# Kernel optimization log

Measured on AMD Instinct MI355X. Metric: run time of the kernel, lower is better.

Reference implementation:

```python
import jax, jax.numpy as jnp
import numpy as np

N_HEAD = 16

def setup_inputs() -> dict:
    key = jax.random.key(0)
    k1, k2, k3 = jax.random.split(key, 3)
    B, T, C = 2, 2048, 2048
    x = jax.random.normal(k1, (B, T, C), dtype=jnp.float32)
    # torch Linear weights are [out, in]; init with small scale for stability
    w_attn = jax.random.normal(k2, (3 * C, C), dtype=jnp.float32) * 0.02
    b_attn = jnp.zeros((3 * C,), dtype=jnp.float32)
    w_proj = jax.random.normal(k3, (C, C), dtype=jnp.float32) * 0.02
    b_proj = jnp.zeros((C,), dtype=jnp.float32)
    return {"x": x, "w_attn": w_attn, "b_attn": b_attn, "w_proj": w_proj, "b_proj": b_proj}

def reference(x, w_attn, b_attn, w_proj, b_proj):
    B, T, C = x.shape
    nh = N_HEAD
    hs = C // nh
    # fused QKV projection (torch Linear: x @ W^T + b)
    qkv = x @ w_attn.T + b_attn                      # [B, T, 3C]
    q, k, v = jnp.split(qkv, 3, axis=2)
    # [B, nh, T, hs]
    q = q.reshape(B, T, nh, hs).transpose(0, 2, 1, 3)
    k = k.reshape(B, T, nh, hs).transpose(0, 2, 1, 3)
    v = v.reshape(B, T, nh, hs).transpose(0, 2, 1, 3)
    # causal scaled dot-product attention
    scale = 1.0 / jnp.sqrt(jnp.asarray(hs, dtype=x.dtype))
    logits = jnp.einsum("bhqd,bhkd->bhqk", q, k) * scale  # [B, nh, T, T]
    causal = jnp.tril(jnp.ones((T, T), dtype=bool))
    logits = jnp.where(causal, logits, jnp.finfo(logits.dtype).min)
    attn = jax.nn.softmax(logits, axis=-1)
    y = jnp.einsum("bhqk,bhkd->bhqd", attn, v)       # [B, nh, T, hs]
    y = y.transpose(0, 2, 1, 3).reshape(B, T, C)
    # output projection (resid_dropout is identity in eval / p=0)
    y = y @ w_proj.T + b_proj
    return y
```

## Files before the change

### kernel.cpp

```cpp
#include <hip/hip_runtime.h>
#include <stdint.h>

typedef __bf16 bf16_t;
typedef __bf16 bf16x8 __attribute__((ext_vector_type(8)));
typedef float f32x4 __attribute__((ext_vector_type(4)));
typedef unsigned short us16x8 __attribute__((ext_vector_type(8)));

#define MFMA16(a, b, c) __builtin_amdgcn_mfma_f32_16x16x32_bf16(a, b, c, 0, 0, 0)
#define BAR() __builtin_amdgcn_s_barrier()
#define PRIO1() __builtin_amdgcn_s_setprio(1)
#define PRIO0() __builtin_amdgcn_s_setprio(0)
#define LGKM0()                                        \
  do {                                                 \
    asm volatile("s_waitcnt lgkmcnt(0)" ::: "memory"); \
    __builtin_amdgcn_sched_barrier(0);                 \
  } while (0)
#define VMCNT(n)                                          \
  do {                                                    \
    asm volatile("s_waitcnt vmcnt(" #n ")" ::: "memory"); \
    __builtin_amdgcn_sched_barrier(0);                    \
  } while (0)

__device__ __forceinline__ void stage16(const bf16_t* g, bf16_t* l) {
  __builtin_amdgcn_global_load_lds((__attribute__((address_space(1))) void*)g,
                                   (__attribute__((address_space(3))) void*)l, 16, 0, 0);
}

__global__ __launch_bounds__(256) void cvt_f32_to_bf16(const float* __restrict__ in,
                                                       bf16_t* __restrict__ out, int n8) {
  int i = blockIdx.x * 256 + threadIdx.x;
  if (i >= n8) return;
  const f32x4* p = (const f32x4*)(in + (size_t)i * 8);
  f32x4 a = p[0], b = p[1];
  bf16x8 o;
  o[0] = (bf16_t)a[0]; o[1] = (bf16_t)a[1]; o[2] = (bf16_t)a[2]; o[3] = (bf16_t)a[3];
  o[4] = (bf16_t)b[0]; o[5] = (bf16_t)b[1]; o[6] = (bf16_t)b[2]; o[7] = (bf16_t)b[3];
  *(bf16x8*)(out + (size_t)i * 8) = o;
}

template <int OUT_BF16>
__global__ __launch_bounds__(512, 2) void gemm_nt_p2(const bf16_t* __restrict__ A,
                                                     const bf16_t* __restrict__ B,
                                                     const float* __restrict__ bias,
                                                     void* __restrict__ Cout,
                                                     int M, int N, int K) {
  __shared__ bf16_t SA[2 * 2 * 256 * 32];
  __shared__ bf16_t SB[2 * 2 * 128 * 32];
  const int tid = threadIdx.x;
  const int l = tid & 63, w = tid >> 6;
  const int l15 = l & 15, l4 = l >> 4;
  const int wm = w >> 1, wn = w & 1;
  const int nbm = M >> 8;
  const int nwg = gridDim.x;
  const int bid = blockIdx.x;
  const int wg = (bid & 7) * (nwg >> 3) + (bid >> 3);
  const int bn = wg / nbm, bm = wg % nbm;

  const int sA0 = tid, sA1 = 512 + tid;
  const int rA0 = sA0 >> 2, rA1 = sA1 >> 2, rB = tid >> 2;
  const int cA0 = ((sA0 & 3) ^ ((rA0 >> 1) & 3)) << 3;
  const int cA1 = ((sA1 & 3) ^ ((rA1 >> 1) & 3)) << 3;
  const int cB = ((tid & 3) ^ ((rB >> 1) & 3)) << 3;
  const bf16_t* gA0 = A + (size_t)(bm * 256 + rA0) * K + cA0;
  const bf16_t* gA1 = A + (size_t)(bm * 256 + rA1) * K + cA1;
  const bf16_t* gB = B + (size_t)(bn * 128 + rB) * K + cB;

  int aoff[4], boff[4];
#pragma unroll
  for (int mi = 0; mi < 4; ++mi) {
    int r = wm * 64 + mi * 16 + l15;
    aoff[mi] = r * 32 + ((l4 ^ ((r >> 1) & 3)) << 3);
  }
#pragma unroll
  for (int ni = 0; ni < 4; ++ni) {
    int r = wn * 64 + ni * 16 + l15;
    boff[ni] = r * 32 + ((l4 ^ ((r >> 1) & 3)) << 3);
  }

  f32x4 acc[4][4] = {};

  auto STAGE = [&](int tau, int h, int buf) {
    const int koff = tau * 64 + h * 32;
    stage16(gA0 + koff, SA + buf * 16384 + h * 8192 + sA0 * 8);
    stage16(gA1 + koff, SA + buf * 16384 + h * 8192 + sA1 * 8);
    stage16(gB + koff, SB + buf * 8192 + h * 4096 + tid * 8);
  };

  auto PHASE = [&](int buf, int h, int tauS, int hS, int bufS) {
    bf16x8 aR[4], bR[4];
#pragma unroll
    for (int mi = 0; mi < 4; ++mi)
      aR[mi] = *(const bf16x8*)(SA + buf * 16384 + h * 8192 + aoff[mi]);
#pragma unroll
    for (int ni = 0; ni < 4; ++ni)
      bR[ni] = *(const bf16x8*)(SB + buf * 8192 + h * 4096 + boff[ni]);
    STAGE(tauS, hS, bufS);
    VMCNT(6);
    BAR();
    LGKM0();
    PRIO1();
#pragma unroll
    for (int mi = 0; mi < 4; ++mi)
#pragma unroll
      for (int ni = 0; ni < 4; ++ni) acc[mi][ni] = MFMA16(aR[mi], bR[ni], acc[mi][ni]);
    PRIO0();
    BAR();
  };

  const int nk = K >> 6;
  STAGE(0, 0, 0);
  STAGE(0, 1, 0);
  STAGE(1, 0, 1);
  VMCNT(6);
  BAR();

  for (int t = 0; t < nk; t += 2) {
    const int t1a = (t + 1 < nk) ? t + 1 : nk - 1;
    const int t2a = (t + 2 < nk) ? t + 2 : nk - 1;
    const int t3a = (t + 3 < nk) ? t + 3 : nk - 1;
    PHASE(0, 0, t1a, 1, 1);
    PHASE(0, 1, t2a, 0, 0);
    PHASE(1, 0, t2a, 1, 0);
    PHASE(1, 1, t3a, 0, 1);
  }
  VMCNT(0);

  const int rbase = bm * 256 + wm * 64 + (l4 << 2);
  const int cbase = bn * 128 + wn * 64 + l15;
#pragma unroll
  for (int ni = 0; ni < 4; ++ni) {
    float bv = bias[cbase + ni * 16];
#pragma unroll
    for (int mi = 0; mi < 4; ++mi)
#pragma unroll
      for (int r = 0; r < 4; ++r) {
        float v = acc[mi][ni][r] + bv;
        size_t off = (size_t)(rbase + mi * 16 + r) * N + (cbase + ni * 16);
        if (OUT_BF16) ((bf16_t*)Cout)[off] = (bf16_t)v;
        else ((float*)Cout)[off] = v;
      }
  }
}

__global__ __launch_bounds__(256, 2) void attn_fwd(const bf16_t* __restrict__ qkv,
                                                   bf16_t* __restrict__ att) {
  __shared__ bf16_t Kt[64 * 128];
  __shared__ bf16_t Vt[128 * 64];
  __shared__ bf16_t Pw[4][16 * 64];

  int bid = blockIdx.x;
  int pair = bid >> 5, bh = bid & 31;
  int h = bh & 15, b = bh >> 4;
  int tid = threadIdx.x;
  int l = tid & 63, w = tid >> 6;
  int l15 = l & 15, l4 = l >> 4, l7 = l & 7;
  const size_t LD = 6144;
  const bf16_t* base = qkv + (size_t)b * 2048 * LD;

#pragma unroll 1
  for (int phase = 0; phase < 2; ++phase) {
    int qt = phase ? 31 - pair : pair;
    int q0 = qt << 6;
    int wq0 = q0 + w * 16;

    bf16x8 qf[4];
#pragma unroll
    for (int kk = 0; kk < 4; ++kk)
      qf[kk] = *(const bf16x8*)(base + (size_t)(wq0 + l15) * LD + h * 128 + kk * 32 + l4 * 8);

    f32x4 acc[8] = {};
    float mrow[4], lrow[4];
#pragma unroll
    for (int r = 0; r < 4; ++r) { mrow[r] = -1e30f; lrow[r] = 0.f; }

    int nkt = qt + 1;
    for (int kt = 0; kt < nkt; ++kt) {
      int kb = kt << 6;
      const bf16_t* vg = base + (size_t)kb * LD + 4096 + h * 128;
      us16x8 va[2], vb[2];
#pragma unroll
      for (int p = 0; p < 2; ++p) {
        int g = p * 256 + tid;
        int kv = (g >> 4) << 1;
        int d0 = (g & 15) << 3;
        va[p] = *(const us16x8*)(vg + (size_t)kv * LD + d0);
        vb[p] = *(const us16x8*)(vg + (size_t)(kv + 1) * LD + d0);
      }
      const bf16_t* kg = base + (size_t)kb * LD + 2048 + h * 128;
#pragma unroll
      for (int i = 0; i < 4; ++i) {
        int e = i * 256 + tid;
        int row = e >> 4, blk = e & 15;
        int src = (blk ^ (row & 7)) << 3;
        stage16(kg + (size_t)row * LD + src, Kt + e * 8);
      }
#pragma unroll
      for (int p = 0; p < 2; ++p) {
        int g = p * 256 + tid;
        int kv = (g >> 4) << 1;
        int d0 = (g & 15) << 3;
        int k8 = kv >> 3, kr = kv & 7;
#pragma unroll
        for (int j = 0; j < 8; ++j) {
          int d = d0 + j;
          int swz = k8 ^ ((d ^ (d >> 3)) & 7);
          unsigned pack = (unsigned)va[p][j] | ((unsigned)vb[p][j] << 16);
          *(unsigned*)(&Vt[d * 64 + swz * 8 + kr]) = pack;
        }
      }
      __syncthreads();

      {
        f32x4 s[4] = {};
        __builtin_amdgcn_s_setprio(1);
#pragma unroll
        for (int kk = 0; kk < 4; ++kk) {
          int blk = (kk * 4 + l4) ^ l7;
#pragma unroll
          for (int n = 0; n < 4; ++n) {
            bf16x8 kf = *(const bf16x8*)(Kt + (n * 16 + l15) * 128 + blk * 8);
            s[n] = MFMA16(qf[kk], kf, s[n]);
          }
        }
        __builtin_amdgcn_s_setprio(0);

        const float sc = 0.08838834764831845f;
        bool needMask = (kb + 63) > wq0;
        float scf[4];
#pragma unroll
        for (int r = 0; r < 4; ++r) {
          int q = wq0 + (l4 << 2) + r;
#pragma unroll
          for (int n = 0; n < 4; ++n) {
            float v = s[n][r] * sc;
            if (needMask && (kb + n * 16 + l15) > q) v = -1e30f;
            s[n][r] = v;
          }
          float mx = fmaxf(fmaxf(s[0][r], s[1][r]), fmaxf(s[2][r], s[3][r]));
          mx = fmaxf(mx, __shfl_xor(mx, 1));
          mx = fmaxf(mx, __shfl_xor(mx, 2));
          mx = fmaxf(mx, __shfl_xor(mx, 4));
          mx = fmaxf(mx, __shfl_xor(mx, 8));
          float mn = fmaxf(mrow[r], mx);
          float sf = __expf(mrow[r] - mn);
          mrow[r] = mn;
          scf[r] = sf;
          float rs = 0.f;
#pragma unroll
          for (int n = 0; n < 4; ++n) {
            float pv = __expf(s[n][r] - mn);
            s[n][r] = pv;
            rs += pv;
          }
          rs += __shfl_xor(rs, 1);
          rs += __shfl_xor(rs, 2);
          rs += __shfl_xor(rs, 4);
          rs += __shfl_xor(rs, 8);
          lrow[r] = lrow[r] * sf + rs;
        }
#pragma unroll
        for (int nd = 0; nd < 8; ++nd)
#pragma unroll
          for (int r = 0; r < 4; ++r)
            acc[nd][r] *= scf[r];
#pragma unroll
        for (int n = 0; n < 4; ++n) {
          int cb8 = n * 2 + (l15 >> 3);
#pragma unroll
          for (int r = 0; r < 4; ++r) {
            int row = (l4 << 2) + r;
            Pw[w][row * 64 + ((cb8 ^ (row & 7)) << 3) + l7] = (bf16_t)s[n][r];
          }
        }
        __builtin_amdgcn_s_setprio(1);
#pragma unroll
        for (int kk2 = 0; kk2 < 2; ++kk2) {
          bf16x8 pa = *(const bf16x8*)(&Pw[w][l15 * 64 + (((kk2 * 4 + l4) ^ l7) << 3)]);
#pragma unroll
          for (int nd = 0; nd < 8; ++nd) {
            int d = nd * 16 + l15;
            int swz = (kk2 * 4 + l4) ^ ((d ^ (d >> 3)) & 7);
            bf16x8 bv = *(const bf16x8*)(&Vt[d * 64 + swz * 8]);
            acc[nd] = MFMA16(pa, bv, acc[nd]);
          }
        }
        __builtin_amdgcn_s_setprio(0);
      }
      __syncthreads();
    }

#pragma unroll
    for (int r = 0; r < 4; ++r) {
      float inv = 1.0f / lrow[r];
      size_t ro = (size_t)(b * 2048 + wq0 + (l4 << 2) + r) * 2048 + h * 128;
#pragma unroll
      for (int nd = 0; nd < 8; ++nd)
        att[ro + nd * 16 + l15] = (bf16_t)(acc[nd][r] * inv);
    }
  }
}

extern "C" void kernel_launch(void* const* d_in, const int* in_sizes, int n_in,
                              void* d_out, int out_size, void* d_ws, size_t ws_size,
                              hipStream_t stream) {
  (void)in_sizes; (void)n_in; (void)out_size; (void)ws_size;
  const float* x = (const float*)d_in[0];
  const float* w_attn = (const float*)d_in[1];
  const float* b_attn = (const float*)d_in[2];
  const float* w_proj = (const float*)d_in[3];
  const float* b_proj = (const float*)d_in[4];
  float* out = (float*)d_out;

  char* ws = (char*)d_ws;
  bf16_t* xb  = (bf16_t*)(ws);
  bf16_t* wab = (bf16_t*)(ws + 16777216);
  bf16_t* wpb = (bf16_t*)(ws + 41943040);
  bf16_t* qkv = (bf16_t*)(ws + 50331648);
  bf16_t* att = xb;

  cvt_f32_to_bf16<<<4096, 256, 0, stream>>>(x, xb, 1048576);
  cvt_f32_to_bf16<<<6144, 256, 0, stream>>>(w_attn, wab, 1572864);
  cvt_f32_to_bf16<<<2048, 256, 0, stream>>>(w_proj, wpb, 524288);

  gemm_nt_p2<1><<<768, 512, 0, stream>>>(xb, wab, b_attn, qkv, 4096, 6144, 2048);

  attn_fwd<<<512, 256, 0, stream>>>(qkv, att);

  gemm_nt_p2<0><<<256, 512, 0, stream>>>(att, wpb, b_proj, out, 4096, 2048, 2048);
}
```

Baseline: 310.0 us.

## Replace GEMM with 128x128-tile, 256-thread kernel using quadrant-phased MFMA schedule

Swaps the 256x128-tile, 512-thread GEMM for a 128x128-tile, 256-thread kernel with BK=32 double buffering. Each K-tile is split into four MFMA quadrant phases, with LDS reads and global-to-LDS staging interleaved between them. The smaller tiles double the workgroup count and cut LDS use, so three blocks can share a CU and occupancy and load balance should improve. In exchange there is less data reuse per tile and more barriers per K step. The LDS swizzle is also dropped, which may add bank conflicts.

```diff
diff --git a/kernel.cpp b/kernel.cpp
--- a/kernel.cpp
+++ b/kernel.cpp
@@ -39,93 +39,111 @@
 }
 
 template <int OUT_BF16>
-__global__ __launch_bounds__(512, 2) void gemm_nt_p2(const bf16_t* __restrict__ A,
+__global__ __launch_bounds__(256, 3) void gemm_nt_c4(const bf16_t* __restrict__ A,
                                                      const bf16_t* __restrict__ B,
                                                      const float* __restrict__ bias,
                                                      void* __restrict__ Cout,
                                                      int M, int N, int K) {
-  __shared__ bf16_t SA[2 * 2 * 256 * 32];
-  __shared__ bf16_t SB[2 * 2 * 128 * 32];
+  __shared__ bf16_t SA[2 * 2 * 64 * 32];
+  __shared__ bf16_t SB[2 * 2 * 64 * 32];
   const int tid = threadIdx.x;
   const int l = tid & 63, w = tid >> 6;
   const int l15 = l & 15, l4 = l >> 4;
   const int wm = w >> 1, wn = w & 1;
-  const int nbm = M >> 8;
+  const int nbm = M >> 7;
   const int nwg = gridDim.x;
   const int bid = blockIdx.x;
   const int wg = (bid & 7) * (nwg >> 3) + (bid >> 3);
   const int bn = wg / nbm, bm = wg % nbm;
 
-  const int sA0 = tid, sA1 = 512 + tid;
-  const int rA0 = sA0 >> 2, rA1 = sA1 >> 2, rB = tid >> 2;
-  const int cA0 = ((sA0 & 3) ^ ((rA0 >> 1) & 3)) << 3;
-  const int cA1 = ((sA1 & 3) ^ ((rA1 >> 1) & 3)) << 3;
-  const int cB = ((tid & 3) ^ ((rB >> 1) & 3)) << 3;
-  const bf16_t* gA0 = A + (size_t)(bm * 256 + rA0) * K + cA0;
-  const bf16_t* gA1 = A + (size_t)(bm * 256 + rA1) * K + cA1;
-  const bf16_t* gB = B + (size_t)(bn * 128 + rB) * K + cB;
-
-  int aoff[4], boff[4];
-#pragma unroll
-  for (int mi = 0; mi < 4; ++mi) {
-    int r = wm * 64 + mi * 16 + l15;
-    aoff[mi] = r * 32 + ((l4 ^ ((r >> 1) & 3)) << 3);
-  }
-#pragma unroll
-  for (int ni = 0; ni < 4; ++ni) {
-    int r = wn * 64 + ni * 16 + l15;
-    boff[ni] = r * 32 + ((l4 ^ ((r >> 1) & 3)) << 3);
-  }
+  const int srow = tid >> 2, scol = (tid & 3) << 3;
+  const bf16_t* gA0 = A + (size_t)(bm * 128 + srow) * K + scol;
+  const bf16_t* gA1 = gA0 + (size_t)64 * K;
+  const bf16_t* gB0 = B + (size_t)(bn * 128 + srow) * K + scol;
+  const bf16_t* gB1 = gB0 + (size_t)64 * K;
+  const int aBase = wm * 2048 + l15 * 32 + l4 * 8;
+  const int bBase = wn * 2048 + l15 * 32 + l4 * 8;
 
   f32x4 acc[4][4] = {};
-
-  auto STAGE = [&](int tau, int h, int buf) {
-    const int koff = tau * 64 + h * 32;
-    stage16(gA0 + koff, SA + buf * 16384 + h * 8192 + sA0 * 8);
-    stage16(gA1 + koff, SA + buf * 16384 + h * 8192 + sA1 * 8);
-    stage16(gB + koff, SB + buf * 8192 + h * 4096 + tid * 8);
+  bf16x8 aR[2], bR[4];
+
+  const int nk = K >> 5;
+
+  auto stageB = [&](int t2, int buf) {
+    stage16(gB0 + (size_t)t2 * 32, SB + buf * 4096 + tid * 8);
+    stage16(gB1 + (size_t)t2 * 32, SB + buf * 4096 + 2048 + tid * 8);
   };
-
-  auto PHASE = [&](int buf, int h, int tauS, int hS, int bufS) {
-    bf16x8 aR[4], bR[4];
-#pragma unroll
-    for (int mi = 0; mi < 4; ++mi)
-      aR[mi] = *(const bf16x8*)(SA + buf * 16384 + h * 8192 + aoff[mi]);
-#pragma unroll
-    for (int ni = 0; ni < 4; ++ni)
-      bR[ni] = *(const bf16x8*)(SB + buf * 8192 + h * 4096 + boff[ni]);
-    STAGE(tauS, hS, bufS);
-    VMCNT(6);
+  auto stageA = [&](int t2, int buf) {
+    stage16(gA0 + (size_t)t2 * 32, SA + buf * 4096 + tid * 8);
+    stage16(gA1 + (size_t)t2 * 32, SA + buf * 4096 + 2048 + tid * 8);
+  };
+
+  auto TILE = [&](int buf, int t) {
+    const int t2 = (t + 2 < nk) ? t + 2 : nk - 1;
+    const bf16_t* SAb = SA + buf * 4096;
+    const bf16_t* SBb = SB + buf * 4096;
+    aR[0] = *(const bf16x8*)(SAb + aBase);
+    aR[1] = *(const bf16x8*)(SAb + aBase + 512);
+    bR[0] = *(const bf16x8*)(SBb + bBase);
+    bR[1] = *(const bf16x8*)(SBb + bBase + 512);
     BAR();
     LGKM0();
     PRIO1();
-#pragma unroll
-    for (int mi = 0; mi < 4; ++mi)
-#pragma unroll
-      for (int ni = 0; ni < 4; ++ni) acc[mi][ni] = MFMA16(aR[mi], bR[ni], acc[mi][ni]);
+    acc[0][0] = MFMA16(aR[0], bR[0], acc[0][0]);
+    acc[0][1] = MFMA16(aR[0], bR[1], acc[0][1]);
+    acc[1][0] = MFMA16(aR[1], bR[0], acc[1][0]);
+    acc[1][1] = MFMA16(aR[1], bR[1], acc[1][1]);
     PRIO0();
     BAR();
+    bR[2] = *(const bf16x8*)(SBb + bBase + 1024);
+    bR[3] = *(const bf16x8*)(SBb + bBase + 1536);
+    BAR();
+    LGKM0();
+    PRIO1();
+    acc[0][2] = MFMA16(aR[0], bR[2], acc[0][2]);
+    acc[0][3] = MFMA16(aR[0], bR[3], acc[0][3]);
+    acc[1][2] = MFMA16(aR[1], bR[2], acc[1][2]);
+    acc[1][3] = MFMA16(aR[1], bR[3], acc[1][3]);
+    PRIO0();
+    BAR();
+    aR[0] = *(const bf16x8*)(SAb + aBase + 1024);
+    aR[1] = *(const bf16x8*)(SAb + aBase + 1536);
+    stageB(t2, buf);
+    BAR();
+    LGKM0();
+    PRIO1();
+    acc[2][2] = MFMA16(aR[0], bR[2], acc[2][2]);
+    acc[2][3] = MFMA16(aR[0], bR[3], acc[2][3]);
+    acc[3][2] = MFMA16(aR[1], bR[2], acc[3][2]);
+    acc[3][3] = MFMA16(aR[1], bR[3], acc[3][3]);
+    PRIO0();
+    BAR();
+    stageA(t2, buf);
+    VMCNT(4);
+    BAR();
+    PRIO1();
+    acc[2][0] = MFMA16(aR[0], bR[0], acc[2][0]);
+    acc[2][1] = MFMA16(aR[0], bR[1], acc[2][1]);
+    acc[3][0] = MFMA16(aR[1], bR[0], acc[3][0]);
+    acc[3][1] = MFMA16(aR[1], bR[1], acc[3][1]);
+    PRIO0();
+    BAR();
   };
 
-  const int nk = K >> 6;
-  STAGE(0, 0, 0);
-  STAGE(0, 1, 0);
-  STAGE(1, 0, 1);
-  VMCNT(6);
+  stageB(0, 0);
+  stageA(0, 0);
+  stageB(1, 1);
+  stageA(1, 1);
+  VMCNT(4);
   BAR();
 
   for (int t = 0; t < nk; t += 2) {
-    const int t1a = (t + 1 < nk) ? t + 1 : nk - 1;
-    const int t2a = (t + 2 < nk) ? t + 2 : nk - 1;
-    const int t3a = (t + 3 < nk) ? t + 3 : nk - 1;
-    PHASE(0, 0, t1a, 1, 1);
-    PHASE(0, 1, t2a, 0, 0);
-    PHASE(1, 0, t2a, 1, 0);
-    PHASE(1, 1, t3a, 0, 1);
+    TILE(0, t);
+    TILE(1, t + 1);
   }
   VMCNT(0);
 
-  const int rbase = bm * 256 + wm * 64 + (l4 << 2);
+  const int rbase = bm * 128 + wm * 64 + (l4 << 2);
   const int cbase = bn * 128 + wn * 64 + l15;
 #pragma unroll
   for (int ni = 0; ni < 4; ++ni) {
@@ -322,9 +340,9 @@
   cvt_f32_to_bf16<<<6144, 256, 0, stream>>>(w_attn, wab, 1572864);
   cvt_f32_to_bf16<<<2048, 256, 0, stream>>>(w_proj, wpb, 524288);
 
-  gemm_nt_p2<1><<<768, 512, 0, stream>>>(xb, wab, b_attn, qkv, 4096, 6144, 2048);
+  gemm_nt_c4<1><<<1536, 256, 0, stream>>>(xb, wab, b_attn, qkv, 4096, 6144, 2048);
 
   attn_fwd<<<512, 256, 0, stream>>>(qkv, att);
 
-  gemm_nt_p2<0><<<256, 512, 0, stream>>>(att, wpb, b_proj, out, 4096, 2048, 2048);
-}
+  gemm_nt_c4<0><<<512, 256, 0, stream>>>(att, wpb, b_proj, out, 4096, 2048, 2048);
+}
```

Measured after the change: 295.2 us. 4.8% less time.

## Replace 256x128 double-buffered GEMM with 128x128 triple-buffered 256-thread GEMM

Applied to the files above, without the earlier changes.

Both projection GEMMs now use 128x128 block tiles with 256 threads and K-steps of 32. A three-slot LDS ring replaces the old two-buffer, two-half-phase schedule, and launch bounds allow three blocks per CU. The aim is more concurrent blocks and finer-grained load/compute overlap, which matters most for the output projection that previously launched only 256 blocks. The trade-off is smaller tiles, which give less operand reuse per global load and more barriers per unit of K.

```diff
diff --git a/kernel.cpp b/kernel.cpp
--- a/kernel.cpp
+++ b/kernel.cpp
@@ -39,93 +39,84 @@
 }
 
 template <int OUT_BF16>
-__global__ __launch_bounds__(512, 2) void gemm_nt_p2(const bf16_t* __restrict__ A,
-                                                     const bf16_t* __restrict__ B,
-                                                     const float* __restrict__ bias,
-                                                     void* __restrict__ Cout,
-                                                     int M, int N, int K) {
-  __shared__ bf16_t SA[2 * 2 * 256 * 32];
-  __shared__ bf16_t SB[2 * 2 * 128 * 32];
+__global__ __launch_bounds__(256, 3) void gemm_tb3(const bf16_t* __restrict__ A,
+                                                   const bf16_t* __restrict__ B,
+                                                   const float* __restrict__ bias,
+                                                   void* __restrict__ Cout,
+                                                   int M, int N, int K) {
+  __shared__ bf16_t SA[3 * 128 * 32];
+  __shared__ bf16_t SB[3 * 128 * 32];
   const int tid = threadIdx.x;
   const int l = tid & 63, w = tid >> 6;
   const int l15 = l & 15, l4 = l >> 4;
   const int wm = w >> 1, wn = w & 1;
-  const int nbm = M >> 8;
+  const int nbm = M >> 7;
   const int nwg = gridDim.x;
   const int bid = blockIdx.x;
   const int wg = (bid & 7) * (nwg >> 3) + (bid >> 3);
   const int bn = wg / nbm, bm = wg % nbm;
 
-  const int sA0 = tid, sA1 = 512 + tid;
-  const int rA0 = sA0 >> 2, rA1 = sA1 >> 2, rB = tid >> 2;
-  const int cA0 = ((sA0 & 3) ^ ((rA0 >> 1) & 3)) << 3;
-  const int cA1 = ((sA1 & 3) ^ ((rA1 >> 1) & 3)) << 3;
-  const int cB = ((tid & 3) ^ ((rB >> 1) & 3)) << 3;
-  const bf16_t* gA0 = A + (size_t)(bm * 256 + rA0) * K + cA0;
-  const bf16_t* gA1 = A + (size_t)(bm * 256 + rA1) * K + cA1;
-  const bf16_t* gB = B + (size_t)(bn * 128 + rB) * K + cB;
-
+  const int r0 = tid >> 2;
+  const int sc = (((tid & 3) ^ ((r0 >> 1) & 3)) << 3);
+  const bf16_t* gA = A + (size_t)(bm * 128 + r0) * K + sc;
+  const bf16_t* gB = B + (size_t)(bn * 128 + r0) * K + sc;
+  const size_t rowK64 = (size_t)64 * K;
+
+  const int swz = (l4 ^ ((l15 >> 1) & 3)) << 3;
   int aoff[4], boff[4];
 #pragma unroll
-  for (int mi = 0; mi < 4; ++mi) {
-    int r = wm * 64 + mi * 16 + l15;
-    aoff[mi] = r * 32 + ((l4 ^ ((r >> 1) & 3)) << 3);
+  for (int i = 0; i < 4; ++i) {
+    aoff[i] = (wm * 64 + i * 16 + l15) * 32 + swz;
+    boff[i] = (wn * 64 + i * 16 + l15) * 32 + swz;
   }
-#pragma unroll
-  for (int ni = 0; ni < 4; ++ni) {
-    int r = wn * 64 + ni * 16 + l15;
-    boff[ni] = r * 32 + ((l4 ^ ((r >> 1) & 3)) << 3);
-  }
 
   f32x4 acc[4][4] = {};
-
-  auto STAGE = [&](int tau, int h, int buf) {
-    const int koff = tau * 64 + h * 32;
-    stage16(gA0 + koff, SA + buf * 16384 + h * 8192 + sA0 * 8);
-    stage16(gA1 + koff, SA + buf * 16384 + h * 8192 + sA1 * 8);
-    stage16(gB + koff, SB + buf * 8192 + h * 4096 + tid * 8);
+  const int nk = K >> 5;
+
+  auto STAGE = [&](int t2, int buf) {
+    const size_t ko = (size_t)t2 * 32;
+    stage16(gA + ko, SA + buf * 4096 + tid * 8);
+    stage16(gA + rowK64 + ko, SA + buf * 4096 + 2048 + tid * 8);
+    stage16(gB + ko, SB + buf * 4096 + tid * 8);
+    stage16(gB + rowK64 + ko, SB + buf * 4096 + 2048 + tid * 8);
   };
 
-  auto PHASE = [&](int buf, int h, int tauS, int hS, int bufS) {
+  auto TILE = [&](int t, int bufR, int bufS) {
+    const int t2 = (t + 2 < nk) ? t + 2 : nk - 1;
+    STAGE(t2, bufS);
     bf16x8 aR[4], bR[4];
 #pragma unroll
-    for (int mi = 0; mi < 4; ++mi)
-      aR[mi] = *(const bf16x8*)(SA + buf * 16384 + h * 8192 + aoff[mi]);
-#pragma unroll
-    for (int ni = 0; ni < 4; ++ni)
-      bR[ni] = *(const bf16x8*)(SB + buf * 8192 + h * 4096 + boff[ni]);
-    STAGE(tauS, hS, bufS);
-    VMCNT(6);
+    for (int i = 0; i < 4; ++i) {
+      aR[i] = *(const bf16x8*)(SA + bufR * 4096 + aoff[i]);
+      bR[i] = *(const bf16x8*)(SB + bufR * 4096 + boff[i]);
+    }
+    VMCNT(4);
     BAR();
     LGKM0();
     PRIO1();
 #pragma unroll
     for (int mi = 0; mi < 4; ++mi)
 #pragma unroll
-      for (int ni = 0; ni < 4; ++ni) acc[mi][ni] = MFMA16(aR[mi], bR[ni], acc[mi][ni]);
+      for (int ni = 0; ni < 4; ++ni)
+        acc[mi][ni] = MFMA16(aR[mi], bR[ni], acc[mi][ni]);
     PRIO0();
     BAR();
   };
 
-  const int nk = K >> 6;
-  STAGE(0, 0, 0);
-  STAGE(0, 1, 0);
-  STAGE(1, 0, 1);
-  VMCNT(6);
+  STAGE(0, 0);
+  STAGE(1, 1);
+  VMCNT(4);
   BAR();
 
-  for (int t = 0; t < nk; t += 2) {
-    const int t1a = (t + 1 < nk) ? t + 1 : nk - 1;
-    const int t2a = (t + 2 < nk) ? t + 2 : nk - 1;
-    const int t3a = (t + 3 < nk) ? t + 3 : nk - 1;
-    PHASE(0, 0, t1a, 1, 1);
-    PHASE(0, 1, t2a, 0, 0);
-    PHASE(1, 0, t2a, 1, 0);
-    PHASE(1, 1, t3a, 0, 1);
+  for (int t = 0; t < nk - 1; t += 3) {
+    TILE(t, 0, 2);
+    TILE(t + 1, 1, 0);
+    TILE(t + 2, 2, 1);
   }
+  TILE(nk - 1, 0, 2);
   VMCNT(0);
 
-  const int rbase = bm * 256 + wm * 64 + (l4 << 2);
+  const int rbase = bm * 128 + wm * 64 + (l4 << 2);
   const int cbase = bn * 128 + wn * 64 + l15;
 #pragma unroll
   for (int ni = 0; ni < 4; ++ni) {
@@ -322,9 +313,9 @@
   cvt_f32_to_bf16<<<6144, 256, 0, stream>>>(w_attn, wab, 1572864);
   cvt_f32_to_bf16<<<2048, 256, 0, stream>>>(w_proj, wpb, 524288);
 
-  gemm_nt_p2<1><<<768, 512, 0, stream>>>(xb, wab, b_attn, qkv, 4096, 6144, 2048);
+  gemm_tb3<1><<<1536, 256, 0, stream>>>(xb, wab, b_attn, qkv, 4096, 6144, 2048);
 
   attn_fwd<<<512, 256, 0, stream>>>(qkv, att);
 
-  gemm_nt_p2<0><<<256, 512, 0, stream>>>(att, wpb, b_proj, out, 4096, 2048, 2048);
-}
+  gemm_tb3<0><<<512, 256, 0, stream>>>(att, wpb, b_proj, out, 4096, 2048, 2048);
+}
```

Result: faster. 299.1 us (-3.5%).
